# Kernel optimization log

Measured on AMD Instinct MI355X. Metric: run time of the kernel, lower is better.

Reference implementation:

```python
import jax, jax.numpy as jnp
import numpy as np

N_NODES = 100000
N_EDGES = 1600000
IN_FEAT = 64
HIDDEN = 64
OUT_FEAT = 64
FCHIDDEN = 32
EMB_DIM = 20
FINAL_DIM = 2


def gcn_conv(x, W, b, src, dst, num_nodes):
    """PyG-style GCNConv: add self-loops, symmetric norm, linear, scatter-add."""
    loop = jnp.arange(num_nodes)
    s = jnp.concatenate([src, loop])  # message sources (x_j)
    d = jnp.concatenate([dst, loop])  # aggregation targets
    ones = jnp.ones(s.shape[0], dtype=x.dtype)
    deg = jax.ops.segment_sum(ones, d, num_segments=num_nodes)
    dinv = jnp.where(deg > 0, jax.lax.rsqrt(jnp.maximum(deg, 1.0)), 0.0)
    norm = dinv[s] * dinv[d]                      # [E+N]
    h = x @ W                                     # [N, out]
    msg = h[s] * norm[:, None]                    # gather + scale
    return jax.ops.segment_sum(msg, d, num_segments=num_nodes) + b


def setup_inputs() -> dict:
    key = jax.random.key(0)
    ks = jax.random.split(key, 12)
    x = jax.random.normal(ks[0], (N_NODES, IN_FEAT), dtype=jnp.float32)
    edge_index = jax.random.randint(ks[1], (2, N_EDGES), 0, N_NODES, dtype=jnp.int64)
    edge_attr = jax.random.randint(ks[2], (4, N_EDGES), 0, EMB_DIM, dtype=jnp.int64)
    def lin(k, fan_in, fan_out):
        bound = 1.0 / np.sqrt(fan_in)
        kw, kb = jax.random.split(k)
        W = jax.random.uniform(kw, (fan_in, fan_out), jnp.float32, -bound, bound)
        b = jax.random.uniform(kb, (fan_out,), jnp.float32, -bound, bound)
        return W, b
    W1, b1 = lin(ks[3], IN_FEAT, HIDDEN)
    W2, b2 = lin(ks[4], HIDDEN, OUT_FEAT)
    emb0 = jax.random.normal(ks[5], (EMB_DIM, FCHIDDEN), dtype=jnp.float32)
    emb1 = jax.random.normal(ks[6], (EMB_DIM, FCHIDDEN), dtype=jnp.float32)
    fc_in = OUT_FEAT + 2 * FCHIDDEN + 2
    fcW1, fcb1 = lin(ks[7], fc_in, FINAL_DIM)
    fcW2, fcb2 = lin(ks[8], FINAL_DIM, 2)
    return dict(x=x, edge_index=edge_index, edge_attr=edge_attr,
                W1=W1, b1=b1, W2=W2, b2=b2, emb0=emb0, emb1=emb1,
                fcW1=fcW1, fcb1=fcb1, fcW2=fcW2, fcb2=fcb2)


def reference(x, edge_index, edge_attr, W1, b1, W2, b2, emb0, emb1,
              fcW1, fcb1, fcW2, fcb2):
    num_nodes = x.shape[0]
    src, dst = edge_index[0], edge_index[1]
    h = jax.nn.relu(gcn_conv(x, W1, b1, src, dst, num_nodes))
    h = gcn_conv(h, W2, b2, src, dst, num_nodes)
    node2edge = h[src] - h[dst]                     # [E, outFeat]
    ea = edge_attr.T                                # [E, 4]
    vl = ea[:, :2].astype(jnp.float32)              # [E, 2]
    e0 = emb0[ea[:, 2]]                             # [E, fchidden]
    e1 = emb1[ea[:, 3]]                             # [E, fchidden]
    total = jnp.concatenate([node2edge, vl, e0, e1], axis=1)
    out = jax.nn.relu(total @ fcW1 + fcb1)          # dropout = identity (eval)
    out = out @ fcW2 + fcb2                         # [E, 2]
    return jax.nn.log_softmax(out, axis=1)
```

## Files before the change

### kernel.cpp

```cpp
#include <hip/hip_runtime.h>
#include <hip/hip_bf16.h>
#include <math.h>


typedef __hip_bfloat16 bf16;
#define NBLK 256

__global__ __launch_bounds__(256) void kA(const int* __restrict__ dst,
                                          int* __restrict__ cntm,
                                          int E, int chunk, int NB) {
    __shared__ int h[512];
    int blk = blockIdx.x;
    for (int i = threadIdx.x; i < NB; i += 256) h[i] = 0;
    __syncthreads();
    int lo = blk * chunk, hi = min(E, lo + chunk);
    for (int e = lo + threadIdx.x; e < hi; e += 256)
        atomicAdd(&h[dst[e] >> 8], 1);
    __syncthreads();
    for (int i = threadIdx.x; i < NB; i += 256)
        cntm[(size_t)i * NBLK + blk] = h[i];
}

__global__ void k_mscan1(int* __restrict__ a, int* __restrict__ part, int M) {
    __shared__ int s[256];
    int i = blockIdx.x * 256 + threadIdx.x;
    int v = (i < M) ? a[i] : 0;
    s[threadIdx.x] = v;
    int x = v;
    for (int off = 1; off < 256; off <<= 1) {
        __syncthreads();
        int add = (threadIdx.x >= off) ? s[threadIdx.x - off] : 0;
        __syncthreads();
        x += add;
        s[threadIdx.x] = x;
    }
    if (i < M) a[i] = x - v;
    __syncthreads();
    if (threadIdx.x == 255) part[blockIdx.x] = s[255];
}

__global__ void k_scan2(int* __restrict__ part, int B) {
    __shared__ int s[512];
    int t = threadIdx.x;
    int v = (t < B) ? part[t] : 0;
    s[t] = v;
    int x = v;
    for (int off = 1; off < 512; off <<= 1) {
        __syncthreads();
        int add = (t >= off) ? s[t - off] : 0;
        __syncthreads();
        x += add;
        s[t] = x;
    }
    if (t < B) part[t] = x - v;
}

__global__ void k_mscan3(int* __restrict__ a, const int* __restrict__ part, int M) {
    int i = blockIdx.x * 256 + threadIdx.x;
    if (i < M) a[i] += part[blockIdx.x];
}

__global__ __launch_bounds__(256) void kB(const int* __restrict__ src,
                                          const int* __restrict__ dst,
                                          const int* __restrict__ cntm,
                                          int* __restrict__ pairs,
                                          int E, int chunk, int NB) {
    __shared__ int off[512];
    int blk = blockIdx.x;
    for (int i = threadIdx.x; i < NB; i += 256)
        off[i] = cntm[(size_t)i * NBLK + blk];
    __syncthreads();
    int lo = blk * chunk, hi = min(E, lo + chunk);
    for (int e = lo + threadIdx.x; e < hi; e += 256) {
        int d = dst[e];
        int pos = atomicAdd(&off[d >> 8], 1);
        pairs[pos] = ((d & 255) << 17) | src[e];
    }
}

__global__ __launch_bounds__(256) void kC(const int* __restrict__ cntm,
                                          const int* __restrict__ pairs,
                                          int* __restrict__ col, int* __restrict__ rp,
                                          float* __restrict__ dinv,
                                          int N, int E, int NB) {
    __shared__ int cnt[256];
    __shared__ int s[256];
    int b = blockIdx.x, t = threadIdx.x;
    int n0 = b << 8;
    int nn = min(256, N - n0);
    int base = cntm[(size_t)b * NBLK];
    int end  = (b == NB - 1) ? E : cntm[(size_t)(b + 1) * NBLK];
    cnt[t] = 0;
    __syncthreads();
    for (int j = base + t; j < end; j += 256)
        atomicAdd(&cnt[pairs[j] >> 17], 1);
    __syncthreads();
    int v = cnt[t];
    if (t < nn) dinv[n0 + t] = rsqrtf((float)v + 1.0f);
    s[t] = v;
    int x = v;
    for (int off = 1; off < 256; off <<= 1) {
        __syncthreads();
        int add = (t >= off) ? s[t - off] : 0;
        __syncthreads();
        x += add;
        s[t] = x;
    }
    __syncthreads();
    int excl = x - v;
    if (t < nn) rp[n0 + t] = base + excl;
    cnt[t] = base + excl;
    __syncthreads();
    for (int j = base + t; j < end; j += 256) {
        int v2 = pairs[j];
        int pos = atomicAdd(&cnt[v2 >> 17], 1);
        col[pos] = v2 & 0x1FFFF;
    }
    if (b == NB - 1 && t == 0) rp[N] = E;
}

__global__ void k_small(const float* __restrict__ W2,
                        const float* __restrict__ emb0, const float* __restrict__ emb1,
                        const float* __restrict__ fcW1, const float* __restrict__ fcb1,
                        const float* __restrict__ fcW2, const float* __restrict__ fcb2,
                        float* __restrict__ U, float* __restrict__ E0t,
                        float* __restrict__ E1t, float* __restrict__ C) {
    int t = threadIdx.x;
    for (int c = 0; c < 2; ++c) {
        float s = 0.f;
        for (int j = 0; j < 64; ++j) s += W2[t * 64 + j] * fcW1[j * 2 + c];
        U[t * 2 + c] = s;
    }
    if (t < 20) {
        for (int c = 0; c < 2; ++c) {
            float s0 = 0.f, s1 = 0.f;
            for (int k = 0; k < 32; ++k) {
                s0 += emb0[t * 32 + k] * fcW1[(66 + k) * 2 + c];
                s1 += emb1[t * 32 + k] * fcW1[(98 + k) * 2 + c];
            }
            E0t[t * 2 + c] = s0;
            E1t[t * 2 + c] = s1;
        }
    }
    if (t == 0) {
        C[0] = fcb1[0];
        C[1] = fcb1[1];
        C[2] = fcW1[64 * 2 + 0]; C[3] = fcW1[64 * 2 + 1];
        C[4] = fcW1[65 * 2 + 0]; C[5] = fcW1[65 * 2 + 1];
        C[6] = fcW2[0]; C[7] = fcW2[1];
        C[8] = fcW2[2]; C[9] = fcW2[3];
        C[10] = fcb2[0]; C[11] = fcb2[1];
    }
}

__global__ __launch_bounds__(256) void k_gemm1(const float* __restrict__ x,
                                               const float* __restrict__ W1,
                                               bf16* __restrict__ xW, int N) {
    __shared__ __align__(16) float xs[64][68];
    __shared__ __align__(16) float Ws[64][64];
    int tid = threadIdx.x;
    int n0 = blockIdx.x * 64;
    for (int i = tid; i < 4096; i += 256) Ws[i >> 6][i & 63] = W1[i];
    for (int i = tid; i < 4096; i += 256) {
        int node = i >> 6, k = i & 63;
        float v = (n0 + node < N) ? x[(size_t)(n0 + node) * 64 + k] : 0.f;
        xs[k][node] = v;
    }
    __syncthreads();
    int tr = tid >> 4;
    int tc = tid & 15;
    float acc[4][4] = {};
#pragma unroll 8
    for (int k = 0; k < 64; ++k) {
        float4 xv = *(const float4*)&xs[k][tr * 4];
        float4 wv = *(const float4*)&Ws[k][tc * 4];
        acc[0][0] = fmaf(xv.x, wv.x, acc[0][0]);
        acc[0][1] = fmaf(xv.x, wv.y, acc[0][1]);
        acc[0][2] = fmaf(xv.x, wv.z, acc[0][2]);
        acc[0][3] = fmaf(xv.x, wv.w, acc[0][3]);
        acc[1][0] = fmaf(xv.y, wv.x, acc[1][0]);
        acc[1][1] = fmaf(xv.y, wv.y, acc[1][1]);
        acc[1][2] = fmaf(xv.y, wv.z, acc[1][2]);
        acc[1][3] = fmaf(xv.y, wv.w, acc[1][3]);
        acc[2][0] = fmaf(xv.z, wv.x, acc[2][0]);
        acc[2][1] = fmaf(xv.z, wv.y, acc[2][1]);
        acc[2][2] = fmaf(xv.z, wv.z, acc[2][2]);
        acc[2][3] = fmaf(xv.z, wv.w, acc[2][3]);
        acc[3][0] = fmaf(xv.w, wv.x, acc[3][0]);
        acc[3][1] = fmaf(xv.w, wv.y, acc[3][1]);
        acc[3][2] = fmaf(xv.w, wv.z, acc[3][2]);
        acc[3][3] = fmaf(xv.w, wv.w, acc[3][3]);
    }
#pragma unroll
    for (int i = 0; i < 4; ++i) {
        int node = n0 + tr * 4 + i;
        if (node < N) {
            __hip_bfloat162 p0, p1;
            p0.x = __float2bfloat16(acc[i][0]);
            p0.y = __float2bfloat16(acc[i][1]);
            p1.x = __float2bfloat16(acc[i][2]);
            p1.y = __float2bfloat16(acc[i][3]);
            __hip_bfloat162* dst2 = (__hip_bfloat162*)&xW[(size_t)node * 64 + tc * 4];
            dst2[0] = p0;
            dst2[1] = p1;
        }
    }
}

__global__ __launch_bounds__(256) void k_gather1(
        const bf16* __restrict__ xW, const float* __restrict__ dinv,
        const int* __restrict__ rp, const int* __restrict__ col,
        const float* __restrict__ b1, const float* __restrict__ U,
        float* __restrict__ Q, float* __restrict__ P, int N, int E) {
    int wid = (blockIdx.x * 256 + threadIdx.x) >> 6;
    int o = threadIdx.x & 63;
    if (wid >= N) return;
    float di = dinv[wid];
    float acc = di * __bfloat162float(xW[(size_t)wid * 64 + o]);
    int beg = rp[wid], end = rp[wid + 1];
    for (int base = beg; base < end; base += 64) {
        int nn = min(64, end - base);
        int colv = col[min(base + o, E - 1)];
        int jj = 0;
        for (; jj + 8 <= nn; jj += 8) {
            int m0 = __shfl(colv, jj + 0);
            int m1 = __shfl(colv, jj + 1);
            int m2 = __shfl(colv, jj + 2);
            int m3 = __shfl(colv, jj + 3);
            int m4 = __shfl(colv, jj + 4);
            int m5 = __shfl(colv, jj + 5);
            int m6 = __shfl(colv, jj + 6);
            int m7 = __shfl(colv, jj + 7);
            float w0 = dinv[m0], w1 = dinv[m1], w2 = dinv[m2], w3 = dinv[m3];
            float w4 = dinv[m4], w5 = dinv[m5], w6 = dinv[m6], w7 = dinv[m7];
            float v0 = __bfloat162float(xW[(size_t)m0 * 64 + o]);
            float v1 = __bfloat162float(xW[(size_t)m1 * 64 + o]);
            float v2 = __bfloat162float(xW[(size_t)m2 * 64 + o]);
            float v3 = __bfloat162float(xW[(size_t)m3 * 64 + o]);
            float v4 = __bfloat162float(xW[(size_t)m4 * 64 + o]);
            float v5 = __bfloat162float(xW[(size_t)m5 * 64 + o]);
            float v6 = __bfloat162float(xW[(size_t)m6 * 64 + o]);
            float v7 = __bfloat162float(xW[(size_t)m7 * 64 + o]);
            acc = fmaf(w0, v0, acc);
            acc = fmaf(w1, v1, acc);
            acc = fmaf(w2, v2, acc);
            acc = fmaf(w3, v3, acc);
            acc = fmaf(w4, v4, acc);
            acc = fmaf(w5, v5, acc);
            acc = fmaf(w6, v6, acc);
            acc = fmaf(w7, v7, acc);
        }
        for (; jj < nn; ++jj) {
            int m = __shfl(colv, jj);
            acc = fmaf(dinv[m], __bfloat162float(xW[(size_t)m * 64 + o]), acc);
        }
    }
    acc *= di;
    float h = fmaxf(acc + b1[o], 0.f);
    float q0 = h * U[o * 2 + 0];
    float q1 = h * U[o * 2 + 1];
#pragma unroll
    for (int mm = 32; mm; mm >>= 1) {
        q0 += __shfl_xor(q0, mm);
        q1 += __shfl_xor(q1, mm);
    }
    if (o == 0) {
        float d2 = di * di;
        Q[2 * wid + 0] = q0;      Q[2 * wid + 1] = q1;
        P[2 * wid + 0] = d2 * q0; P[2 * wid + 1] = d2 * q1;
    }
}

__global__ void k_gather2(const float* __restrict__ dinv, const int* __restrict__ rp,
                          const int* __restrict__ col, const float* __restrict__ Q,
                          float* __restrict__ P, int N) {
    int n = blockIdx.x * blockDim.x + threadIdx.x;
    if (n >= N) return;
    float di = dinv[n];
    float p0 = P[2 * n + 0], p1 = P[2 * n + 1];
    int beg = rp[n], end = rp[n + 1];
    for (int j = beg; j < end; ++j) {
        int m = col[j];
        float w = di * dinv[m];
        float2 q = ((const float2*)Q)[m];
        p0 = fmaf(w, q.x, p0);
        p1 = fmaf(w, q.y, p1);
    }
    P[2 * n + 0] = p0;
    P[2 * n + 1] = p1;
}

__global__ void k_edge(const int* __restrict__ src, const int* __restrict__ dst,
                       const int* __restrict__ attr, const float* __restrict__ P,
                       const float* __restrict__ E0t, const float* __restrict__ E1t,
                       const float* __restrict__ C, float* __restrict__ out, int E) {
    int e = blockIdx.x * blockDim.x + threadIdx.x;
    if (e >= E) return;
    int s = src[e], d = dst[e];
    float a0 = (float)attr[e];
    float a1 = (float)attr[E + e];
    int i2 = attr[2 * E + e], i3 = attr[3 * E + e];
    const float2* P2 = (const float2*)P;
    float2 ps = P2[s], pd = P2[d];
    float z0 = ps.x - pd.x + a0 * C[2] + a1 * C[4] + E0t[i2 * 2 + 0] + E1t[i3 * 2 + 0] + C[0];
    float z1 = ps.y - pd.y + a0 * C[3] + a1 * C[5] + E0t[i2 * 2 + 1] + E1t[i3 * 2 + 1] + C[1];
    float r0 = fmaxf(z0, 0.f), r1 = fmaxf(z1, 0.f);
    float o0 = r0 * C[6] + r1 * C[8] + C[10];
    float o1 = r0 * C[7] + r1 * C[9] + C[11];
    float m = fmaxf(o0, o1);
    float lse = m + logf(expf(o0 - m) + expf(o1 - m));
    float2 res;
    res.x = o0 - lse;
    res.y = o1 - lse;
    ((float2*)out)[e] = res;
}

extern "C" void kernel_launch(void* const* d_in, const int* in_sizes, int n_in,
                              void* d_out, int out_size, void* d_ws, size_t ws_size,
                              hipStream_t stream) {
    const float* x    = (const float*)d_in[0];
    const int*   ei   = (const int*)d_in[1];
    const int*   ea   = (const int*)d_in[2];
    const float* W1   = (const float*)d_in[3];
    const float* b1   = (const float*)d_in[4];
    const float* W2   = (const float*)d_in[5];
    const float* emb0 = (const float*)d_in[7];
    const float* emb1 = (const float*)d_in[8];
    const float* fcW1 = (const float*)d_in[9];
    const float* fcb1 = (const float*)d_in[10];
    const float* fcW2 = (const float*)d_in[11];
    const float* fcb2 = (const float*)d_in[12];

    const int N = in_sizes[0] / 64;
    const int E = in_sizes[1] / 2;
    const int* src = ei;
    const int* dst = ei + E;
    const int NB = (N + 255) >> 8;
    const int NBB = NB * NBLK;
    const int chunk = (E + NBLK - 1) / NBLK;
    const int BS = (NBB + 255) / 256;

    char* wsb = (char*)d_ws;
    float* dinv = (float*)wsb;
    int*   rp   = (int*)(wsb + (size_t)4 * 100352);
    int*   cntm = (int*)(wsb + (size_t)4 * 200704);
    int*   part = (int*)(wsb + (size_t)4 * 300800);
    float* U    = (float*)(wsb + (size_t)4 * 301312);
    float* E0t  = U + 128;
    float* E1t  = E0t + 40;
    float* C    = E1t + 40;
    float* Q    = (float*)(wsb + (size_t)4 * 301568);
    float* P    = (float*)(wsb + (size_t)4 * 501760);
    bf16*  xW   = (bf16*)(wsb + (size_t)4 * 702464);
    int*   col   = (int*)d_out;
    int*   pairs = (int*)d_out + E;

    k_small<<<1, 64, 0, stream>>>(W2, emb0, emb1, fcW1, fcb1, fcW2, fcb2,
                                  U, E0t, E1t, C);
    kA<<<NBLK, 256, 0, stream>>>(dst, cntm, E, chunk, NB);
    k_mscan1<<<BS, 256, 0, stream>>>(cntm, part, NBB);
    k_scan2<<<1, 512, 0, stream>>>(part, BS);
    k_mscan3<<<BS, 256, 0, stream>>>(cntm, part, NBB);
    kB<<<NBLK, 256, 0, stream>>>(src, dst, cntm, pairs, E, chunk, NB);
    kC<<<NB, 256, 0, stream>>>(cntm, pairs, col, rp, dinv, N, E, NB);
    k_gemm1<<<(N + 63) / 64, 256, 0, stream>>>(x, W1, xW, N);
    k_gather1<<<((size_t)N * 64 + 255) / 256, 256, 0, stream>>>(xW, dinv, rp, col, b1, U, Q, P, N, E);
    k_gather2<<<(N + 255) / 256, 256, 0, stream>>>(dinv, rp, col, Q, P, N);
    k_edge<<<(E + 255) / 256, 256, 0, stream>>>(src, dst, ea, P, E0t, E1t, C,
                                                (float*)d_out, E);
}
```

Measured before the change: 297.6 us.

## Aggregate per destination bucket in shared memory instead of building full CSR

Drops the second counting-sort pass (kC), so the row pointers and column arrays are no longer built. Both GCN aggregations now run directly over the 256-node bucketed pairs, using shared-memory float atomics per block. The source-side dinv scaling is folded into the GEMM output, so the gather needs no per-neighbour dinv load. The trade-off is that kE launches only about 391 blocks, each with 64KB of shared memory, which limits occupancy and parallelism, and it relies on LDS float atomics.

Result: slower. 996.2 us (+234.7%).

```diff
diff --git a/kernel.cpp b/kernel.cpp
--- a/kernel.cpp
+++ b/kernel.cpp
@@ -78,16 +78,12 @@
     }
 }
 
-__global__ __launch_bounds__(256) void kC(const int* __restrict__ cntm,
+__global__ __launch_bounds__(256) void kD(const int* __restrict__ cntm,
                                           const int* __restrict__ pairs,
-                                          int* __restrict__ col, int* __restrict__ rp,
                                           float* __restrict__ dinv,
                                           int N, int E, int NB) {
     __shared__ int cnt[256];
-    __shared__ int s[256];
     int b = blockIdx.x, t = threadIdx.x;
-    int n0 = b << 8;
-    int nn = min(256, N - n0);
     int base = cntm[(size_t)b * NBLK];
     int end  = (b == NB - 1) ? E : cntm[(size_t)(b + 1) * NBLK];
     cnt[t] = 0;
@@ -95,28 +91,8 @@
     for (int j = base + t; j < end; j += 256)
         atomicAdd(&cnt[pairs[j] >> 17], 1);
     __syncthreads();
-    int v = cnt[t];
-    if (t < nn) dinv[n0 + t] = rsqrtf((float)v + 1.0f);
-    s[t] = v;
-    int x = v;
-    for (int off = 1; off < 256; off <<= 1) {
-        __syncthreads();
-        int add = (t >= off) ? s[t - off] : 0;
-        __syncthreads();
-        x += add;
-        s[t] = x;
-    }
-    __syncthreads();
-    int excl = x - v;
-    if (t < nn) rp[n0 + t] = base + excl;
-    cnt[t] = base + excl;
-    __syncthreads();
-    for (int j = base + t; j < end; j += 256) {
-        int v2 = pairs[j];
-        int pos = atomicAdd(&cnt[v2 >> 17], 1);
-        col[pos] = v2 & 0x1FFFF;
-    }
-    if (b == NB - 1 && t == 0) rp[N] = E;
+    int n = (b << 8) + t;
+    if (n < N) dinv[n] = rsqrtf((float)cnt[t] + 1.0f);
 }
 
 __global__ void k_small(const float* __restrict__ W2,
@@ -155,7 +131,8 @@
 
 __global__ __launch_bounds__(256) void k_gemm1(const float* __restrict__ x,
                                                const float* __restrict__ W1,
-                                               bf16* __restrict__ xW, int N) {
+                                               const float* __restrict__ dinv,
+                                               bf16* __restrict__ xWs, int N) {
     __shared__ __align__(16) float xs[64][68];
     __shared__ __align__(16) float Ws[64][64];
     int tid = threadIdx.x;
@@ -195,99 +172,125 @@
     for (int i = 0; i < 4; ++i) {
         int node = n0 + tr * 4 + i;
         if (node < N) {
+            float di = dinv[node];
             __hip_bfloat162 p0, p1;
-            p0.x = __float2bfloat16(acc[i][0]);
-            p0.y = __float2bfloat16(acc[i][1]);
-            p1.x = __float2bfloat16(acc[i][2]);
-            p1.y = __float2bfloat16(acc[i][3]);
-            __hip_bfloat162* dst2 = (__hip_bfloat162*)&xW[(size_t)node * 64 + tc * 4];
+            p0.x = __float2bfloat16(di * acc[i][0]);
+            p0.y = __float2bfloat16(di * acc[i][1]);
+            p1.x = __float2bfloat16(di * acc[i][2]);
+            p1.y = __float2bfloat16(di * acc[i][3]);
+            __hip_bfloat162* dst2 = (__hip_bfloat162*)&xWs[(size_t)node * 64 + tc * 4];
             dst2[0] = p0;
             dst2[1] = p1;
         }
     }
 }
 
-__global__ __launch_bounds__(256) void k_gather1(
-        const bf16* __restrict__ xW, const float* __restrict__ dinv,
-        const int* __restrict__ rp, const int* __restrict__ col,
-        const float* __restrict__ b1, const float* __restrict__ U,
-        float* __restrict__ Q, float* __restrict__ P, int N, int E) {
-    int wid = (blockIdx.x * 256 + threadIdx.x) >> 6;
-    int o = threadIdx.x & 63;
-    if (wid >= N) return;
-    float di = dinv[wid];
-    float acc = di * __bfloat162float(xW[(size_t)wid * 64 + o]);
-    int beg = rp[wid], end = rp[wid + 1];
-    for (int base = beg; base < end; base += 64) {
-        int nn = min(64, end - base);
-        int colv = col[min(base + o, E - 1)];
+__global__ __launch_bounds__(256) void kE(const bf16* __restrict__ xWs,
+                                          const int* __restrict__ cntm,
+                                          const int* __restrict__ pairs,
+                                          const float* __restrict__ dinv,
+                                          const float* __restrict__ b1,
+                                          const float* __restrict__ U,
+                                          float* __restrict__ Qs,
+                                          int N, int E, int NB) {
+    __shared__ float agg[256 * 64];
+    int t = threadIdx.x, b = blockIdx.x;
+    float4 z4 = {0.f, 0.f, 0.f, 0.f};
+#pragma unroll
+    for (int i = 0; i < 16; ++i)
+        *(float4*)&agg[(i * 256 + t) * 4] = z4;
+    __syncthreads();
+    int base = cntm[(size_t)b * NBLK];
+    int end  = (b == NB - 1) ? E : cntm[(size_t)(b + 1) * NBLK];
+    int o = t & 63;
+    int wv = t >> 6;
+    for (int jb = base + wv * 64; jb < end; jb += 256) {
+        int nn = min(64, end - jb);
+        int pv = pairs[min(jb + o, E - 1)];
         int jj = 0;
         for (; jj + 8 <= nn; jj += 8) {
-            int m0 = __shfl(colv, jj + 0);
-            int m1 = __shfl(colv, jj + 1);
-            int m2 = __shfl(colv, jj + 2);
-            int m3 = __shfl(colv, jj + 3);
-            int m4 = __shfl(colv, jj + 4);
-            int m5 = __shfl(colv, jj + 5);
-            int m6 = __shfl(colv, jj + 6);
-            int m7 = __shfl(colv, jj + 7);
-            float w0 = dinv[m0], w1 = dinv[m1], w2 = dinv[m2], w3 = dinv[m3];
-            float w4 = dinv[m4], w5 = dinv[m5], w6 = dinv[m6], w7 = dinv[m7];
-            float v0 = __bfloat162float(xW[(size_t)m0 * 64 + o]);
-            float v1 = __bfloat162float(xW[(size_t)m1 * 64 + o]);
-            float v2 = __bfloat162float(xW[(size_t)m2 * 64 + o]);
-            float v3 = __bfloat162float(xW[(size_t)m3 * 64 + o]);
-            float v4 = __bfloat162float(xW[(size_t)m4 * 64 + o]);
-            float v5 = __bfloat162float(xW[(size_t)m5 * 64 + o]);
-            float v6 = __bfloat162float(xW[(size_t)m6 * 64 + o]);
-            float v7 = __bfloat162float(xW[(size_t)m7 * 64 + o]);
-            acc = fmaf(w0, v0, acc);
-            acc = fmaf(w1, v1, acc);
-            acc = fmaf(w2, v2, acc);
-            acc = fmaf(w3, v3, acc);
-            acc = fmaf(w4, v4, acc);
-            acc = fmaf(w5, v5, acc);
-            acc = fmaf(w6, v6, acc);
-            acc = fmaf(w7, v7, acc);
+            int p0 = __shfl(pv, jj + 0);
+            int p1 = __shfl(pv, jj + 1);
+            int p2 = __shfl(pv, jj + 2);
+            int p3 = __shfl(pv, jj + 3);
+            int p4 = __shfl(pv, jj + 4);
+            int p5 = __shfl(pv, jj + 5);
+            int p6 = __shfl(pv, jj + 6);
+            int p7 = __shfl(pv, jj + 7);
+            float v0 = __bfloat162float(xWs[(size_t)(p0 & 0x1FFFF) * 64 + o]);
+            float v1 = __bfloat162float(xWs[(size_t)(p1 & 0x1FFFF) * 64 + o]);
+            float v2 = __bfloat162float(xWs[(size_t)(p2 & 0x1FFFF) * 64 + o]);
+            float v3 = __bfloat162float(xWs[(size_t)(p3 & 0x1FFFF) * 64 + o]);
+            float v4 = __bfloat162float(xWs[(size_t)(p4 & 0x1FFFF) * 64 + o]);
+            float v5 = __bfloat162float(xWs[(size_t)(p5 & 0x1FFFF) * 64 + o]);
+            float v6 = __bfloat162float(xWs[(size_t)(p6 & 0x1FFFF) * 64 + o]);
+            float v7 = __bfloat162float(xWs[(size_t)(p7 & 0x1FFFF) * 64 + o]);
+            atomicAdd(&agg[((p0 >> 17) << 6) + o], v0);
+            atomicAdd(&agg[((p1 >> 17) << 6) + o], v1);
+            atomicAdd(&agg[((p2 >> 17) << 6) + o], v2);
+            atomicAdd(&agg[((p3 >> 17) << 6) + o], v3);
+            atomicAdd(&agg[((p4 >> 17) << 6) + o], v4);
+            atomicAdd(&agg[((p5 >> 17) << 6) + o], v5);
+            atomicAdd(&agg[((p6 >> 17) << 6) + o], v6);
+            atomicAdd(&agg[((p7 >> 17) << 6) + o], v7);
         }
         for (; jj < nn; ++jj) {
-            int m = __shfl(colv, jj);
-            acc = fmaf(dinv[m], __bfloat162float(xW[(size_t)m * 64 + o]), acc);
-        }
-    }
-    acc *= di;
-    float h = fmaxf(acc + b1[o], 0.f);
-    float q0 = h * U[o * 2 + 0];
-    float q1 = h * U[o * 2 + 1];
+            int p = __shfl(pv, jj);
+            float v = __bfloat162float(xWs[(size_t)(p & 0x1FFFF) * 64 + o]);
+            atomicAdd(&agg[((p >> 17) << 6) + o], v);
+        }
+    }
+    __syncthreads();
+    for (int i = 0; i < 64; ++i) {
+        int ln = (wv << 6) + i;
+        int n = (b << 8) + ln;
+        if (n >= N) break;
+        float di = dinv[n];
+        float self = __bfloat162float(xWs[(size_t)n * 64 + o]);
+        float a = di * (agg[(ln << 6) + o] + self);
+        float h = fmaxf(a + b1[o], 0.f);
+        float q0 = h * U[o * 2 + 0];
+        float q1 = h * U[o * 2 + 1];
 #pragma unroll
-    for (int mm = 32; mm; mm >>= 1) {
-        q0 += __shfl_xor(q0, mm);
-        q1 += __shfl_xor(q1, mm);
-    }
-    if (o == 0) {
-        float d2 = di * di;
-        Q[2 * wid + 0] = q0;      Q[2 * wid + 1] = q1;
-        P[2 * wid + 0] = d2 * q0; P[2 * wid + 1] = d2 * q1;
-    }
-}
-
-__global__ void k_gather2(const float* __restrict__ dinv, const int* __restrict__ rp,
-                          const int* __restrict__ col, const float* __restrict__ Q,
-                          float* __restrict__ P, int N) {
-    int n = blockIdx.x * blockDim.x + threadIdx.x;
-    if (n >= N) return;
-    float di = dinv[n];
-    float p0 = P[2 * n + 0], p1 = P[2 * n + 1];
-    int beg = rp[n], end = rp[n + 1];
-    for (int j = beg; j < end; ++j) {
-        int m = col[j];
-        float w = di * dinv[m];
-        float2 q = ((const float2*)Q)[m];
-        p0 = fmaf(w, q.x, p0);
-        p1 = fmaf(w, q.y, p1);
-    }
-    P[2 * n + 0] = p0;
-    P[2 * n + 1] = p1;
+        for (int mm = 32; mm; mm >>= 1) {
+            q0 += __shfl_xor(q0, mm);
+            q1 += __shfl_xor(q1, mm);
+        }
+        if (o == 0) {
+            Qs[2 * n + 0] = di * q0;
+            Qs[2 * n + 1] = di * q1;
+        }
+    }
+}
+
+__global__ __launch_bounds__(256) void kC2(const int* __restrict__ cntm,
+                                           const int* __restrict__ pairs,
+                                           const float* __restrict__ Qs,
+                                           const float* __restrict__ dinv,
+                                           float* __restrict__ P,
+                                           int N, int E, int NB) {
+    __shared__ float acc[512];
+    int t = threadIdx.x, b = blockIdx.x;
+    acc[2 * t] = 0.f;
+    acc[2 * t + 1] = 0.f;
+    __syncthreads();
+    int base = cntm[(size_t)b * NBLK];
+    int end  = (b == NB - 1) ? E : cntm[(size_t)(b + 1) * NBLK];
+    for (int j = base + t; j < end; j += 256) {
+        int p = pairs[j];
+        float2 q = ((const float2*)Qs)[p & 0x1FFFF];
+        int ld = p >> 17;
+        atomicAdd(&acc[2 * ld + 0], q.x);
+        atomicAdd(&acc[2 * ld + 1], q.y);
+    }
+    __syncthreads();
+    int n = (b << 8) + t;
+    if (n < N) {
+        float di = dinv[n];
+        float2 qs = ((const float2*)Qs)[n];
+        P[2 * n + 0] = di * (acc[2 * t + 0] + qs.x);
+        P[2 * n + 1] = di * (acc[2 * t + 1] + qs.y);
+    }
 }
 
 __global__ void k_edge(const int* __restrict__ src, const int* __restrict__ dst,
@@ -342,18 +345,16 @@
 
     char* wsb = (char*)d_ws;
     float* dinv = (float*)wsb;
-    int*   rp   = (int*)(wsb + (size_t)4 * 100352);
-    int*   cntm = (int*)(wsb + (size_t)4 * 200704);
-    int*   part = (int*)(wsb + (size_t)4 * 300800);
-    float* U    = (float*)(wsb + (size_t)4 * 301312);
+    int*   cntm = (int*)(wsb + (size_t)4 * 100352);
+    int*   part = (int*)(wsb + (size_t)4 * 200704);
+    float* U    = (float*)(wsb + (size_t)4 * 201216);
     float* E0t  = U + 128;
     float* E1t  = E0t + 40;
     float* C    = E1t + 40;
-    float* Q    = (float*)(wsb + (size_t)4 * 301568);
-    float* P    = (float*)(wsb + (size_t)4 * 501760);
-    bf16*  xW   = (bf16*)(wsb + (size_t)4 * 702464);
-    int*   col   = (int*)d_out;
-    int*   pairs = (int*)d_out + E;
+    float* Qs   = (float*)(wsb + (size_t)4 * 201728);
+    float* P    = (float*)(wsb + (size_t)4 * 402432);
+    bf16*  xWs  = (bf16*)(wsb + (size_t)4 * 603136);
+    int*   pairs = (int*)d_out;
 
     k_small<<<1, 64, 0, stream>>>(W2, emb0, emb1, fcW1, fcb1, fcW2, fcb2,
                                   U, E0t, E1t, C);
@@ -362,10 +363,10 @@
     k_scan2<<<1, 512, 0, stream>>>(part, BS);
     k_mscan3<<<BS, 256, 0, stream>>>(cntm, part, NBB);
     kB<<<NBLK, 256, 0, stream>>>(src, dst, cntm, pairs, E, chunk, NB);
-    kC<<<NB, 256, 0, stream>>>(cntm, pairs, col, rp, dinv, N, E, NB);
-    k_gemm1<<<(N + 63) / 64, 256, 0, stream>>>(x, W1, xW, N);
-    k_gather1<<<((size_t)N * 64 + 255) / 256, 256, 0, stream>>>(xW, dinv, rp, col, b1, U, Q, P, N, E);
-    k_gather2<<<(N + 255) / 256, 256, 0, stream>>>(dinv, rp, col, Q, P, N);
+    kD<<<NB, 256, 0, stream>>>(cntm, pairs, dinv, N, E, NB);
+    k_gemm1<<<(N + 63) / 64, 256, 0, stream>>>(x, W1, dinv, xWs, N);
+    kE<<<NB, 256, 0, stream>>>(xWs, cntm, pairs, dinv, b1, U, Qs, N, E, NB);
+    kC2<<<NB, 256, 0, stream>>>(cntm, pairs, Qs, dinv, P, N, E, NB);
     k_edge<<<(E + 255) / 256, 256, 0, stream>>>(src, dst, ea, P, E0t, E1t, C,
                                                 (float*)d_out, E);
 }
```
